# Kernel optimization log

Hardware: AMD Instinct MI355X
Metric: run time of the kernel (lower is better)

## Reference

```python
import jax, jax.numpy as jnp
import numpy as np
import math


def setup_inputs() -> dict:
    key = jax.random.key(0)
    k1, k2 = jax.random.split(key)
    x = jax.random.normal(k1, (16, 512, 32, 32), dtype=jnp.float32)
    gamma = jax.random.normal(k2, (1,), dtype=jnp.float32)  # learned scale (init 0 in torch; randomized here)
    beta = 0.5 * jnp.ones((1,), dtype=jnp.float32)          # learned blend (init 0.5)
    return {"x": x, "gamma": gamma, "beta": beta}


def reference(x, gamma, beta):
    # x: (B, C, H, W)
    B, C, H, W = x.shape
    N = H * W
    Xf = x.reshape(B, C, N)  # proj_query / proj_value

    # ave_I = (1/N) * (I - (1/N) * ones(N,N)); X @ ave_I == (X - mean_N(X)) / N exactly.
    Xc = Xf - jnp.mean(Xf, axis=2, keepdims=True)
    scale = 1.0 / (N * math.sqrt(N))
    # sigma = proj_query @ ave_I @ proj_key / sqrt(N)  -> (B, C, C)
    sigma = jnp.einsum('bcn,bdn->bcd', Xc, Xf) * scale

    # energy = proj_query @ proj_key  -> (B, C, C)
    energy = jnp.einsum('bcn,bdn->bcd', Xf, Xf)
    energy_new = jnp.max(energy, axis=-1, keepdims=True) - energy

    b = beta[0]
    attention = b * jax.nn.softmax(sigma, axis=-1) + (1.0 - b) * jax.nn.softmax(energy_new, axis=-1)

    out = jnp.einsum('bcd,bdn->bcn', attention, Xf).reshape(B, C, H, W)
    out = gamma[0] * out + x
    return out
```

## Files before the change

### kernel.cpp

```cpp
#include <hip/hip_runtime.h>

typedef unsigned short u16;
typedef _Float16 f16x8 __attribute__((ext_vector_type(8)));
typedef float f32x4 __attribute__((ext_vector_type(4)));

#define AS1 __attribute__((address_space(1)))
#define AS3 __attribute__((address_space(3)))

#define BB 16
#define CC 512
#define NN 1024

__device__ __forceinline__ void async16(void* lds, const void* g) {
  __builtin_amdgcn_global_load_lds((AS1 void*)g, (AS3 void*)lds, 16, 0, 0);
}

__device__ __forceinline__ u16 f2h(float f) {
  _Float16 h = (_Float16)f;
  return __builtin_bit_cast(u16, h);
}

__device__ __forceinline__ float wredSum(float v) {
  for (int m = 32; m >= 1; m >>= 1) v += __shfl_xor(v, m, 64);
  return v;
}
__device__ __forceinline__ float wredMin(float v) {
  for (int m = 32; m >= 1; m >>= 1) v = fminf(v, __shfl_xor(v, m, 64));
  return v;
}
__device__ __forceinline__ float wredMax(float v) {
  for (int m = 32; m >= 1; m >>= 1) v = fmaxf(v, __shfl_xor(v, m, 64));
  return v;
}

template <int ROWS, int T>
__device__ __forceinline__ void stageT(u16* lds, const u16* src, size_t ld, int t) {
#pragma unroll
  for (int i = 0; i < ROWS * 8 / T; ++i) {
    int f = i * T + t;
    int row = f >> 3;
    int c8 = f & 7;
    int sc = (c8 ^ (row & 7)) * 8;
    async16(&lds[(size_t)f * 8], src + (size_t)row * ld + sc);
  }
}

__device__ __forceinline__ f16x8 ldsfrag(const u16* lds, int row, int k0) {
  return *(const f16x8*)&lds[row * 64 + (k0 ^ ((row & 7) * 8))];
}

__global__ __launch_bounds__(256) void k_prepT(const float* __restrict__ x,
                                               u16* __restrict__ xh,
                                               u16* __restrict__ xt,
                                               float* __restrict__ mu) {
  int lid = blockIdx.x;
  int sw = (lid & 7) * 32 + (lid >> 3);
  int b = sw >> 4;
  int c0 = (sw & 15) * 32;
  int t = threadIdx.x;
  int row = t >> 3;
  int col4 = t & 7;
  __shared__ u16 tr[2][64][40];

  const float* xb = x + ((size_t)b * CC + c0) * NN;
  u16* hb = xh + ((size_t)b * CC + c0) * NN;
  u16* tb = xt + (size_t)b * NN * CC + c0;

  float sum = 0.f;
  int wkey = col4 * 4;
  for (int nt = 0; nt < 16; ++nt) {
    u16(*tbuf)[40] = tr[nt & 1];
#pragma unroll
    for (int s = 0; s < 2; ++s) {
      int cc4 = col4 + 8 * s;
      size_t off = (size_t)row * NN + nt * 64 + cc4 * 4;
      float4 v = *(const float4*)&xb[off];
      sum += v.x + v.y + v.z + v.w;
      ushort4 h;
      h.x = f2h(v.x); h.y = f2h(v.y); h.z = f2h(v.z); h.w = f2h(v.w);
      *(ushort4*)&hb[off] = h;
      int csw = row ^ wkey;
      tbuf[cc4 * 4 + 0][csw] = h.x;
      tbuf[cc4 * 4 + 1][csw] = h.y;
      tbuf[cc4 * 4 + 2][csw] = h.z;
      tbuf[cc4 * 4 + 3][csw] = h.w;
    }
    __syncthreads();
    int np = t >> 2, cs = t & 3;
    int rkey = ((np >> 2) & 7) * 4;
#pragma unroll
    for (int s2 = 0; s2 < 2; ++s2) {
      int cl = cs * 4 + s2 * 16;
      *(ushort4*)&tb[(size_t)(nt * 64 + np) * CC + cl] =
          *(ushort4*)&tbuf[np][cl ^ rkey];
    }
  }
  sum += __shfl_xor(sum, 1, 64);
  sum += __shfl_xor(sum, 2, 64);
  sum += __shfl_xor(sum, 4, 64);
  if ((t & 7) == 0) mu[(size_t)b * CC + c0 + row] = sum * (1.0f / (float)NN);
}

__global__ __launch_bounds__(256, 2) void k_gemm1(const u16* __restrict__ xh,
                                                  float* __restrict__ E) {
  int lid = blockIdx.x;
  int sw = (lid & 7) * 32 + (lid >> 3);
  int b = sw >> 4;
  int r = sw & 15;
  int by = r >> 2;
  int bx = r & 3;

  __shared__ u16 lds[2 * 16384];
  int t = threadIdx.x;
  int lane = t & 63, w = t >> 6;
  int wr = (w >> 1) * 64, wc = (w & 1) * 64;
  int fr = lane & 15, fk = (lane >> 4) * 8;

  const u16* Ab = xh + ((size_t)b * CC + by * 128) * NN;
  const u16* Bb = xh + ((size_t)b * CC + bx * 128) * NN;

  f32x4 acc[4][4];
#pragma unroll
  for (int m = 0; m < 4; ++m)
#pragma unroll
    for (int n = 0; n < 4; ++n) acc[m][n] = (f32x4)(0.0f);

  stageT<128, 256>(lds, Ab, NN, t);
  stageT<128, 256>(lds + 8192, Bb, NN, t);
  __syncthreads();

  int cur = 0;
  for (int ks = 0; ks < NN; ks += 64) {
    if (ks + 64 < NN) {
      u16* nb = lds + (cur ^ 1) * 16384;
      stageT<128, 256>(nb, Ab + ks + 64, NN, t);
      stageT<128, 256>(nb + 8192, Bb + ks + 64, NN, t);
    }
    const u16* cb = lds + cur * 16384;
#pragma unroll
    for (int kk = 0; kk < 2; ++kk) {
      f16x8 af[4], bg[4];
#pragma unroll
      for (int m = 0; m < 4; ++m) af[m] = ldsfrag(cb, wr + m * 16 + fr, kk * 32 + fk);
#pragma unroll
      for (int n = 0; n < 4; ++n) bg[n] = ldsfrag(cb + 8192, wc + n * 16 + fr, kk * 32 + fk);
#pragma unroll
      for (int m = 0; m < 4; ++m)
#pragma unroll
        for (int n = 0; n < 4; ++n)
          acc[m][n] = __builtin_amdgcn_mfma_f32_16x16x32_f16(af[m], bg[n], acc[m][n], 0, 0, 0);
    }
    __syncthreads();
    cur ^= 1;
  }

  float* Eb = E + ((size_t)b * CC + by * 128) * CC + bx * 128;
  int orow = wr + (lane >> 4) * 4;
  int ocol = wc + (lane & 15);
#pragma unroll
  for (int m = 0; m < 4; ++m)
#pragma unroll
    for (int n = 0; n < 4; ++n)
#pragma unroll
      for (int q = 0; q < 4; ++q)
        Eb[(size_t)(orow + m * 16 + q) * CC + ocol + n * 16] = acc[m][n][q];
}

__global__ __launch_bounds__(256) void k_att(const float* __restrict__ E,
                                             const float* __restrict__ mu,
                                             const float* __restrict__ beta_p,
                                             u16* __restrict__ att) {
  int lid = blockIdx.x;
  int sw = (lid & 7) * 32 + (lid >> 3);
  int b = sw >> 4;
  int c0 = (sw & 15) * 32;
  int t = threadIdx.x;
  int lane = t & 63, w = t >> 6;
  const float* Eb = E + (size_t)b * CC * CC;
  const float* mub = mu + b * CC;
  float bta = *beta_p;

  for (int i = 0; i < 8; ++i) {
    int c = c0 + w * 8 + i;
    const float* r0 = Eb + (size_t)c * CC;
    float muc = mub[c];

    float e[8], mud[8];
#pragma unroll
    for (int j = 0; j < 8; ++j) {
      int d = lane + j * 64;
      e[j] = r0[d];
      mud[j] = mub[d];
    }
    float emin = fminf(fminf(fminf(e[0], e[1]), fminf(e[2], e[3])),
                       fminf(fminf(e[4], e[5]), fminf(e[6], e[7])));
    emin = wredMin(emin);
    float pe[8], sum_e = 0.f;
#pragma unroll
    for (int j = 0; j < 8; ++j) { pe[j] = __expf(emin - e[j]); sum_e += pe[j]; }
    sum_e = wredSum(sum_e);

    float sg[8];
#pragma unroll
    for (int j = 0; j < 8; ++j)
      sg[j] = (e[j] - (float)NN * muc * mud[j]) * (1.0f / 32768.0f);
    float smax = fmaxf(fmaxf(fmaxf(sg[0], sg[1]), fmaxf(sg[2], sg[3])),
                       fmaxf(fmaxf(sg[4], sg[5]), fmaxf(sg[6], sg[7])));
    smax = wredMax(smax);
    float ps[8], sum_s = 0.f;
#pragma unroll
    for (int j = 0; j < 8; ++j) { ps[j] = __expf(sg[j] - smax); sum_s += ps[j]; }
    sum_s = wredSum(sum_s);

    float we = (1.0f - bta) / sum_e;
    float wsc = bta / sum_s;
    u16* arow = att + ((size_t)b * CC + c) * CC;
#pragma unroll
    for (int j = 0; j < 8; ++j)
      arow[lane + j * 64] = f2h(ps[j] * wsc + pe[j] * we);
  }
}

__global__ __launch_bounds__(256, 2) void k_gemm2(const u16* __restrict__ att,
                                                  const u16* __restrict__ xt,
                                                  const float* __restrict__ x,
                                                  const float* __restrict__ gamma_p,
                                                  float* __restrict__ out) {
  int lid = blockIdx.x;
  int sw = (lid & 7) * 64 + (lid >> 3);
  int b = sw >> 5;
  int r = sw & 31;
  int by = r >> 3;
  int bx = r & 7;

  __shared__ u16 lds[2 * 16384];
  int t = threadIdx.x;
  int lane = t & 63, w = t >> 6;
  int wr = (w >> 1) * 64, wc = (w & 1) * 64;
  int fr = lane & 15, fk = (lane >> 4) * 8;

  const u16* Ab = att + ((size_t)b * CC + by * 128) * CC;
  const u16* Bb = xt + ((size_t)b * NN + bx * 128) * CC;

  f32x4 acc[4][4];
#pragma unroll
  for (int m = 0; m < 4; ++m)
#pragma unroll
    for (int n = 0; n < 4; ++n) acc[m][n] = (f32x4)(0.0f);

  stageT<128, 256>(lds, Ab, CC, t);
  stageT<128, 256>(lds + 8192, Bb, CC, t);
  __syncthreads();

  int cur = 0;
  for (int ks = 0; ks < CC; ks += 64) {
    if (ks + 64 < CC) {
      u16* nb = lds + (cur ^ 1) * 16384;
      stageT<128, 256>(nb, Ab + ks + 64, CC, t);
      stageT<128, 256>(nb + 8192, Bb + ks + 64, CC, t);
    }
    const u16* cb = lds + cur * 16384;
#pragma unroll
    for (int kk = 0; kk < 2; ++kk) {
      f16x8 af[4], bg[4];
#pragma unroll
      for (int m = 0; m < 4; ++m) af[m] = ldsfrag(cb, wr + m * 16 + fr, kk * 32 + fk);
#pragma unroll
      for (int n = 0; n < 4; ++n) bg[n] = ldsfrag(cb + 8192, wc + n * 16 + fr, kk * 32 + fk);
#pragma unroll
      for (int m = 0; m < 4; ++m)
#pragma unroll
        for (int n = 0; n < 4; ++n)
          acc[m][n] = __builtin_amdgcn_mfma_f32_16x16x32_f16(af[m], bg[n], acc[m][n], 0, 0, 0);
    }
    __syncthreads();
    cur ^= 1;
  }

  float g = *gamma_p;
  const float* xb = x + ((size_t)b * CC + by * 128) * NN + bx * 128;
  float* ob = out + ((size_t)b * CC + by * 128) * NN + bx * 128;
  int orow = wr + (lane >> 4) * 4;
  int ocol = wc + (lane & 15);
#pragma unroll
  for (int m = 0; m < 4; ++m)
#pragma unroll
    for (int n = 0; n < 4; ++n)
#pragma unroll
      for (int q = 0; q < 4; ++q) {
        size_t rr = (size_t)(orow + m * 16 + q) * NN + ocol + n * 16;
        ob[rr] = g * acc[m][n][q] + xb[rr];
      }
}

extern "C" void kernel_launch(void* const* d_in, const int* in_sizes, int n_in,
                              void* d_out, int out_size, void* d_ws, size_t ws_size,
                              hipStream_t stream) {
  const float* x = (const float*)d_in[0];
  const float* gamma = (const float*)d_in[1];
  const float* beta = (const float*)d_in[2];
  float* out = (float*)d_out;

  constexpr size_t BCN = (size_t)BB * CC * NN;
  constexpr size_t BCC = (size_t)BB * CC * CC;
  u16* xh = (u16*)d_ws;
  u16* xt = xh + BCN;
  float* mu = (float*)(xt + BCN);
  float* E = mu + (size_t)BB * CC;
  u16* att = xh;

  k_prepT<<<256, 256, 0, stream>>>(x, xh, xt, mu);
  k_gemm1<<<256, 256, 0, stream>>>(xh, E);
  k_att<<<256, 256, 0, stream>>>(E, mu, beta, att);
  k_gemm2<<<512, 256, 0, stream>>>(att, xt, x, gamma, out);
}
```

Before: 69.86 us.

## Fuse energy GEMM with dual softmax and read fp16 residual

Merges the C×C energy GEMM and the attention softmax kernel so each block computes 32 full rows of energy in registers and writes only the fp16 attention. This removes the fp32 energy round trip through global memory and one launch. In exchange, each block stages all 512 channels per K step, which doubles operand loading and limits occupancy to one block per CU. The final residual now reads the fp16 copy of x instead of fp32 input, reducing bandwidth at some precision cost.

```diff
diff --git a/kernel.cpp b/kernel.cpp
--- a/kernel.cpp
+++ b/kernel.cpp
@@ -19,18 +19,8 @@
   _Float16 h = (_Float16)f;
   return __builtin_bit_cast(u16, h);
 }
-
-__device__ __forceinline__ float wredSum(float v) {
-  for (int m = 32; m >= 1; m >>= 1) v += __shfl_xor(v, m, 64);
-  return v;
-}
-__device__ __forceinline__ float wredMin(float v) {
-  for (int m = 32; m >= 1; m >>= 1) v = fminf(v, __shfl_xor(v, m, 64));
-  return v;
-}
-__device__ __forceinline__ float wredMax(float v) {
-  for (int m = 32; m >= 1; m >>= 1) v = fmaxf(v, __shfl_xor(v, m, 64));
-  return v;
+__device__ __forceinline__ float h2f(u16 u) {
+  return (float)__builtin_bit_cast(_Float16, u);
 }
 
 template <int ROWS, int T>
@@ -101,129 +91,161 @@
   if ((t & 7) == 0) mu[(size_t)b * CC + c0 + row] = sum * (1.0f / (float)NN);
 }
 
-__global__ __launch_bounds__(256, 2) void k_gemm1(const u16* __restrict__ xh,
-                                                  float* __restrict__ E) {
-  int lid = blockIdx.x;
-  int sw = (lid & 7) * 32 + (lid >> 3);
-  int b = sw >> 4;
-  int r = sw & 15;
-  int by = r >> 2;
-  int bx = r & 3;
-
-  __shared__ u16 lds[2 * 16384];
-  int t = threadIdx.x;
-  int lane = t & 63, w = t >> 6;
-  int wr = (w >> 1) * 64, wc = (w & 1) * 64;
-  int fr = lane & 15, fk = (lane >> 4) * 8;
-
-  const u16* Ab = xh + ((size_t)b * CC + by * 128) * NN;
-  const u16* Bb = xh + ((size_t)b * CC + bx * 128) * NN;
-
-  f32x4 acc[4][4];
-#pragma unroll
-  for (int m = 0; m < 4; ++m)
-#pragma unroll
-    for (int n = 0; n < 4; ++n) acc[m][n] = (f32x4)(0.0f);
-
-  stageT<128, 256>(lds, Ab, NN, t);
-  stageT<128, 256>(lds + 8192, Bb, NN, t);
-  __syncthreads();
-
-  int cur = 0;
-  for (int ks = 0; ks < NN; ks += 64) {
-    if (ks + 64 < NN) {
-      u16* nb = lds + (cur ^ 1) * 16384;
-      stageT<128, 256>(nb, Ab + ks + 64, NN, t);
-      stageT<128, 256>(nb + 8192, Bb + ks + 64, NN, t);
-    }
-    const u16* cb = lds + cur * 16384;
-#pragma unroll
-    for (int kk = 0; kk < 2; ++kk) {
-      f16x8 af[4], bg[4];
-#pragma unroll
-      for (int m = 0; m < 4; ++m) af[m] = ldsfrag(cb, wr + m * 16 + fr, kk * 32 + fk);
-#pragma unroll
-      for (int n = 0; n < 4; ++n) bg[n] = ldsfrag(cb + 8192, wc + n * 16 + fr, kk * 32 + fk);
-#pragma unroll
-      for (int m = 0; m < 4; ++m)
-#pragma unroll
-        for (int n = 0; n < 4; ++n)
-          acc[m][n] = __builtin_amdgcn_mfma_f32_16x16x32_f16(af[m], bg[n], acc[m][n], 0, 0, 0);
-    }
-    __syncthreads();
-    cur ^= 1;
-  }
-
-  float* Eb = E + ((size_t)b * CC + by * 128) * CC + bx * 128;
-  int orow = wr + (lane >> 4) * 4;
-  int ocol = wc + (lane & 15);
-#pragma unroll
-  for (int m = 0; m < 4; ++m)
-#pragma unroll
-    for (int n = 0; n < 4; ++n)
-#pragma unroll
-      for (int q = 0; q < 4; ++q)
-        Eb[(size_t)(orow + m * 16 + q) * CC + ocol + n * 16] = acc[m][n][q];
-}
-
-__global__ __launch_bounds__(256) void k_att(const float* __restrict__ E,
-                                             const float* __restrict__ mu,
-                                             const float* __restrict__ beta_p,
-                                             u16* __restrict__ att) {
+__global__ __launch_bounds__(256, 1) void k_fused(const u16* __restrict__ xh,
+                                                  const float* __restrict__ mu,
+                                                  const float* __restrict__ beta_p,
+                                                  u16* __restrict__ att) {
   int lid = blockIdx.x;
   int sw = (lid & 7) * 32 + (lid >> 3);
   int b = sw >> 4;
   int c0 = (sw & 15) * 32;
+
+  __shared__ u16 lds[2 * 32768];
+  __shared__ float prA[32][4], prB[32][4];
   int t = threadIdx.x;
   int lane = t & 63, w = t >> 6;
-  const float* Eb = E + (size_t)b * CC * CC;
-  const float* mub = mu + b * CC;
+  int wc = w * 128;
+  int fr = lane & 15, fk = (lane >> 4) * 8;
+
+  const u16* Bb = xh + (size_t)b * CC * NN;
+
+  f32x4 acc[2][8];
+#pragma unroll
+  for (int m = 0; m < 2; ++m)
+#pragma unroll
+    for (int n = 0; n < 8; ++n) acc[m][n] = (f32x4)(0.0f);
+
+  stageT<512, 256>(lds, Bb, NN, t);
+  __syncthreads();
+
+  int cur = 0;
+  for (int ks = 0; ks < NN; ks += 64) {
+    if (ks + 64 < NN) stageT<512, 256>(lds + (cur ^ 1) * 32768, Bb + ks + 64, NN, t);
+    const u16* cb = lds + cur * 32768;
+#pragma unroll
+    for (int kk = 0; kk < 2; ++kk) {
+      f16x8 af[2], bg[8];
+#pragma unroll
+      for (int m = 0; m < 2; ++m) af[m] = ldsfrag(cb, c0 + m * 16 + fr, kk * 32 + fk);
+#pragma unroll
+      for (int n = 0; n < 8; ++n) bg[n] = ldsfrag(cb, wc + n * 16 + fr, kk * 32 + fk);
+#pragma unroll
+      for (int m = 0; m < 2; ++m)
+#pragma unroll
+        for (int n = 0; n < 8; ++n)
+          acc[m][n] = __builtin_amdgcn_mfma_f32_16x16x32_f16(af[m], bg[n], acc[m][n], 0, 0, 0);
+    }
+    __syncthreads();
+    cur ^= 1;
+  }
+
+  const float* mub = mu + (size_t)b * CC;
   float bta = *beta_p;
-
+  float muc_l[2][4], mud_l[8];
+#pragma unroll
+  for (int m = 0; m < 2; ++m)
+#pragma unroll
+    for (int q = 0; q < 4; ++q)
+      muc_l[m][q] = mub[c0 + m * 16 + (lane >> 4) * 4 + q];
+#pragma unroll
+  for (int n = 0; n < 8; ++n) mud_l[n] = mub[wc + n * 16 + fr];
+
+  float eminr[2][4], smaxr[2][4];
+#pragma unroll
+  for (int m = 0; m < 2; ++m)
+#pragma unroll
+    for (int q = 0; q < 4; ++q) {
+      float emin_p = 3.4e38f, smax_p = -3.4e38f;
+#pragma unroll
+      for (int n = 0; n < 8; ++n) {
+        float e = acc[m][n][q];
+        emin_p = fminf(emin_p, e);
+        float sg = (e - 1024.f * muc_l[m][q] * mud_l[n]) * (1.0f / 32768.0f);
+        smax_p = fmaxf(smax_p, sg);
+      }
+#pragma unroll
+      for (int msk = 1; msk <= 8; msk <<= 1) {
+        emin_p = fminf(emin_p, __shfl_xor(emin_p, msk, 64));
+        smax_p = fmaxf(smax_p, __shfl_xor(smax_p, msk, 64));
+      }
+      int r = m * 16 + (lane >> 4) * 4 + q;
+      if ((lane & 15) == 0) { prA[r][w] = emin_p; prB[r][w] = smax_p; }
+    }
+  __syncthreads();
+#pragma unroll
+  for (int m = 0; m < 2; ++m)
+#pragma unroll
+    for (int q = 0; q < 4; ++q) {
+      int r = m * 16 + (lane >> 4) * 4 + q;
+      eminr[m][q] = fminf(fminf(prA[r][0], prA[r][1]), fminf(prA[r][2], prA[r][3]));
+      smaxr[m][q] = fmaxf(fmaxf(prB[r][0], prB[r][1]), fmaxf(prB[r][2], prB[r][3]));
+    }
+  __syncthreads();
+
+  float wer[2][4], wsr[2][4];
+#pragma unroll
+  for (int m = 0; m < 2; ++m)
+#pragma unroll
+    for (int q = 0; q < 4; ++q) {
+      float se_p = 0.f, ss_p = 0.f;
+#pragma unroll
+      for (int n = 0; n < 8; ++n) {
+        float e = acc[m][n][q];
+        se_p += __expf(eminr[m][q] - e);
+        float sg = (e - 1024.f * muc_l[m][q] * mud_l[n]) * (1.0f / 32768.0f);
+        ss_p += __expf(sg - smaxr[m][q]);
+      }
+#pragma unroll
+      for (int msk = 1; msk <= 8; msk <<= 1) {
+        se_p += __shfl_xor(se_p, msk, 64);
+        ss_p += __shfl_xor(ss_p, msk, 64);
+      }
+      int r = m * 16 + (lane >> 4) * 4 + q;
+      if ((lane & 15) == 0) { prA[r][w] = se_p; prB[r][w] = ss_p; }
+    }
+  __syncthreads();
+#pragma unroll
+  for (int m = 0; m < 2; ++m)
+#pragma unroll
+    for (int q = 0; q < 4; ++q) {
+      int r = m * 16 + (lane >> 4) * 4 + q;
+      float se = prA[r][0] + prA[r][1] + prA[r][2] + prA[r][3];
+      float ss = prB[r][0] + prB[r][1] + prB[r][2] + prB[r][3];
+      wer[m][q] = (1.0f - bta) / se;
+      wsr[m][q] = bta / ss;
+    }
+  __syncthreads();
+
+  u16* at = (u16*)lds;
+#pragma unroll
+  for (int m = 0; m < 2; ++m)
+#pragma unroll
+    for (int q = 0; q < 4; ++q) {
+      int r = m * 16 + (lane >> 4) * 4 + q;
+#pragma unroll
+      for (int n = 0; n < 8; ++n) {
+        float e = acc[m][n][q];
+        float pe = __expf(eminr[m][q] - e);
+        float sg = (e - 1024.f * muc_l[m][q] * mud_l[n]) * (1.0f / 32768.0f);
+        float ps = __expf(sg - smaxr[m][q]);
+        at[r * 520 + wc + n * 16 + fr] = f2h(ps * wsr[m][q] + pe * wer[m][q]);
+      }
+    }
+  __syncthreads();
+
+  int row = t >> 3;
+  int colb = (t & 7) * 8;
+  u16* arow = att + ((size_t)b * CC + c0 + row) * CC;
+#pragma unroll
   for (int i = 0; i < 8; ++i) {
-    int c = c0 + w * 8 + i;
-    const float* r0 = Eb + (size_t)c * CC;
-    float muc = mub[c];
-
-    float e[8], mud[8];
-#pragma unroll
-    for (int j = 0; j < 8; ++j) {
-      int d = lane + j * 64;
-      e[j] = r0[d];
-      mud[j] = mub[d];
-    }
-    float emin = fminf(fminf(fminf(e[0], e[1]), fminf(e[2], e[3])),
-                       fminf(fminf(e[4], e[5]), fminf(e[6], e[7])));
-    emin = wredMin(emin);
-    float pe[8], sum_e = 0.f;
-#pragma unroll
-    for (int j = 0; j < 8; ++j) { pe[j] = __expf(emin - e[j]); sum_e += pe[j]; }
-    sum_e = wredSum(sum_e);
-
-    float sg[8];
-#pragma unroll
-    for (int j = 0; j < 8; ++j)
-      sg[j] = (e[j] - (float)NN * muc * mud[j]) * (1.0f / 32768.0f);
-    float smax = fmaxf(fmaxf(fmaxf(sg[0], sg[1]), fmaxf(sg[2], sg[3])),
-                       fmaxf(fmaxf(sg[4], sg[5]), fmaxf(sg[6], sg[7])));
-    smax = wredMax(smax);
-    float ps[8], sum_s = 0.f;
-#pragma unroll
-    for (int j = 0; j < 8; ++j) { ps[j] = __expf(sg[j] - smax); sum_s += ps[j]; }
-    sum_s = wredSum(sum_s);
-
-    float we = (1.0f - bta) / sum_e;
-    float wsc = bta / sum_s;
-    u16* arow = att + ((size_t)b * CC + c) * CC;
-#pragma unroll
-    for (int j = 0; j < 8; ++j)
-      arow[lane + j * 64] = f2h(ps[j] * wsc + pe[j] * we);
+    int col = colb + i * 64;
+    *(uint4*)&arow[col] = *(const uint4*)&at[row * 520 + col];
   }
 }
 
 __global__ __launch_bounds__(256, 2) void k_gemm2(const u16* __restrict__ att,
                                                   const u16* __restrict__ xt,
-                                                  const float* __restrict__ x,
+                                                  const u16* __restrict__ xh,
                                                   const float* __restrict__ gamma_p,
                                                   float* __restrict__ out) {
   int lid = blockIdx.x;
@@ -278,7 +300,7 @@
   }
 
   float g = *gamma_p;
-  const float* xb = x + ((size_t)b * CC + by * 128) * NN + bx * 128;
+  const u16* xb = xh + ((size_t)b * CC + by * 128) * NN + bx * 128;
   float* ob = out + ((size_t)b * CC + by * 128) * NN + bx * 128;
   int orow = wr + (lane >> 4) * 4;
   int ocol = wc + (lane & 15);
@@ -289,7 +311,7 @@
 #pragma unroll
       for (int q = 0; q < 4; ++q) {
         size_t rr = (size_t)(orow + m * 16 + q) * NN + ocol + n * 16;
-        ob[rr] = g * acc[m][n][q] + xb[rr];
+        ob[rr] = g * acc[m][n][q] + h2f(xb[rr]);
       }
 }
 
@@ -306,11 +328,9 @@
   u16* xh = (u16*)d_ws;
   u16* xt = xh + BCN;
   float* mu = (float*)(xt + BCN);
-  float* E = mu + (size_t)BB * CC;
-  u16* att = xh;
+  u16* att = (u16*)(mu + (size_t)BB * CC);
 
   k_prepT<<<256, 256, 0, stream>>>(x, xh, xt, mu);
-  k_gemm1<<<256, 256, 0, stream>>>(xh, E);
-  k_att<<<256, 256, 0, stream>>>(E, mu, beta, att);
-  k_gemm2<<<512, 256, 0, stream>>>(att, xt, x, gamma, out);
-}
+  k_fused<<<256, 256, 0, stream>>>(xh, mu, beta, att);
+  k_gemm2<<<512, 256, 0, stream>>>(att, xt, xh, gamma, out);
+}
```

After: 66.70 us. -4.5%, faster.
